# Optimization experiments

Measured on AMD Instinct MI355X. Metric: run time of the kernel, lower is better.

Reference implementation:

```python
import jax, jax.numpy as jnp
import numpy as np

B, N, M = 64, 4096, 128


def setup_inputs() -> dict:
    key = jax.random.key(0)
    x = jax.random.normal(key, (B, N, M), dtype=jnp.float32)
    return {"x": x}


def reference(x):
    # Original loops over channels M, applying a 1D FFT along the N axis to
    # each (batch, N) slice. Equivalent batched form: FFT along axis=1.
    f = jnp.fft.fft(x.astype(jnp.complex64), axis=1)  # (B, N, M) complex64
    return (jnp.real(f), jnp.imag(f))
```

## Files before the change

### kernel.cpp

```cpp
#include <hip/hip_runtime.h>
#include <hip/hip_fp16.h>

#define B 64
#define N 4096
#define M 128

constexpr int T    = 1024;
constexpr int CPB  = 16;
constexpr int NF   = 8;
constexpr int NWG  = B * (M / CPB);

__device__ __forceinline__ int fold5(int p) {
    return (p & ~31) | ((p ^ (p >> 5) ^ (p >> 9)) & 31);
}
__device__ __forceinline__ int rev12(int k) {
    return ((k & 7) << 9) | (((k >> 3) & 7) << 6) | (((k >> 6) & 7) << 3) | ((k >> 9) & 7);
}

__device__ __forceinline__ float2 cadd(float2 a, float2 b){ return make_float2(a.x+b.x, a.y+b.y); }
__device__ __forceinline__ float2 csub(float2 a, float2 b){ return make_float2(a.x-b.x, a.y-b.y); }
__device__ __forceinline__ float2 cmul(float2 a, float2 b){ return make_float2(a.x*b.x - a.y*b.y, a.x*b.y + a.y*b.x); }
__device__ __forceinline__ float2 mulnegi(float2 a){ return make_float2(a.y, -a.x); }
__device__ __forceinline__ float2 muli(float2 a)  { return make_float2(-a.y, a.x); }
__device__ __forceinline__ float2 cis(float ang){ float s, c; __sincosf(ang, &s, &c); return make_float2(c, s); }
__device__ __forceinline__ float2 h2f(__half2 h){ return __half22float2(h); }
__device__ __forceinline__ __half2 f2h(float2 v){ return __floats2half2_rn(v.x, v.y); }

__device__ __forceinline__ void dft8(float2 t[8]) {
    float2 e0=cadd(t[0],t[4]), e1=csub(t[0],t[4]);
    float2 e2=cadd(t[2],t[6]), e3=csub(t[2],t[6]);
    float2 E0=cadd(e0,e2), E2=csub(e0,e2);
    float2 E1=cadd(e1,mulnegi(e3)), E3=cadd(e1,muli(e3));
    float2 o0=cadd(t[1],t[5]), o1=csub(t[1],t[5]);
    float2 o2=cadd(t[3],t[7]), o3=csub(t[3],t[7]);
    float2 O0=cadd(o0,o2), O2=csub(o0,o2);
    float2 O1=cadd(o1,mulnegi(o3)), O3=cadd(o1,muli(o3));
    const float C = 0.70710678118654752f;
    float2 w1O1 = make_float2(C*(O1.x+O1.y), C*(O1.y-O1.x));
    float2 w2O2 = mulnegi(O2);
    float2 w3O3 = make_float2(C*(O3.y-O3.x), -C*(O3.x+O3.y));
    t[0]=cadd(E0,O0);   t[4]=csub(E0,O0);
    t[1]=cadd(E1,w1O1); t[5]=csub(E1,w1O1);
    t[2]=cadd(E2,w2O2); t[6]=csub(E2,w2O2);
    t[3]=cadd(E3,w3O3); t[7]=csub(E3,w3O3);
}

template<int S>
__device__ __forceinline__ void stage(__half2* z, int tid) {
    #pragma unroll
    for (int it = 0; it < 4; ++it) {
        const int q  = tid + (it << 10);
        const int f  = q >> 9;
        const int qq = q & 511;
        int G, j;
        if      (S == 512) { G = 0;                j = qq;      }
        else if (S == 64)  { G = (qq >> 6) << 9;   j = qq & 63; }
        else if (S == 8)   { G = (qq >> 3) << 6;   j = qq & 7;  }
        else               { G = qq << 3;          j = 0;       }
        const int nbase = G + j;
        const int fb = f << 12;
        int idx[8];
        #pragma unroll
        for (int c = 0; c < 8; ++c) idx[c] = fb + fold5(nbase + c * S);
        float2 r[8];
        #pragma unroll
        for (int c = 0; c < 8; ++c) r[c] = h2f(z[idx[c]]);
        dft8(r);
        if (S > 1) {
            float2 w1 = cis(-6.2831853071795864f * (float)j / (float)(8 * S));
            float2 w = w1;
            #pragma unroll
            for (int k = 1; k < 8; ++k) { r[k] = cmul(r[k], w); w = cmul(w, w1); }
        }
        #pragma unroll
        for (int c = 0; c < 8; ++c) z[idx[c]] = f2h(r[c]);
    }
}

__global__ __launch_bounds__(T, 4)
void fft_one(const float* __restrict__ x, float* __restrict__ out) {
    extern __shared__ __half2 z[];
    const int bid = blockIdx.x;
    const int b = bid >> 3, mg = bid & 7;
    const int m0 = mg * CPB;
    const float* xb = x + (size_t)b * N * M + m0;
    const int tid = threadIdx.x;

    #pragma unroll
    for (int it = 0; it < 16; ++it) {
        int i = tid + (it << 10);
        int n = i >> 2, c = i & 3;
        float4 v = *(const float4*)(xb + (size_t)n * M + (c << 2));
        int fn = fold5(n);
        z[((2 * c)     << 12) + fn] = f2h(make_float2(v.x, v.y));
        z[((2 * c + 1) << 12) + fn] = f2h(make_float2(v.z, v.w));
    }
    __syncthreads();

    stage<512>(z, tid); __syncthreads();
    stage<64 >(z, tid); __syncthreads();
    stage<8  >(z, tid); __syncthreads();
    stage<1  >(z, tid); __syncthreads();

    float* outRe = out;
    float* outIm = out + (size_t)B * N * M;
    const size_t rbase = (size_t)b * N * M + m0;
    #pragma unroll
    for (int it = 0; it < 16; ++it) {
        int u = tid + (it << 10);
        int k = u >> 2, c = u & 3;
        int kk = (N - k) & (N - 1);
        int sk = fold5(rev12(k)), smk = fold5(rev12(kk));
        int f0 = (2 * c) << 12, f1 = (2 * c + 1) << 12;
        float2 Zk0 = h2f(z[f0 + sk]),  Zm0 = h2f(z[f0 + smk]);
        float2 Zk1 = h2f(z[f1 + sk]),  Zm1 = h2f(z[f1 + smk]);
        float4 re, im;
        re.x = 0.5f * (Zk0.x + Zm0.x); im.x = 0.5f * (Zk0.y - Zm0.y);
        re.y = 0.5f * (Zk0.y + Zm0.y); im.y = 0.5f * (Zm0.x - Zk0.x);
        re.z = 0.5f * (Zk1.x + Zm1.x); im.z = 0.5f * (Zk1.y - Zm1.y);
        re.w = 0.5f * (Zk1.y + Zm1.y); im.w = 0.5f * (Zm1.x - Zk1.x);
        *(float4*)(outRe + rbase + (size_t)k * M + (c << 2)) = re;
        *(float4*)(outIm + rbase + (size_t)k * M + (c << 2)) = im;
    }
}

extern "C" void kernel_launch(void* const* d_in, const int* in_sizes, int n_in,
                              void* d_out, int out_size, void* d_ws, size_t ws_size,
                              hipStream_t stream) {
    const float* x = (const float*)d_in[0];
    float* out = (float*)d_out;
    const int lds_bytes = NF * N * (int)sizeof(__half2);
    hipFuncSetAttribute((const void*)fft_one,
                        hipFuncAttributeMaxDynamicSharedMemorySize, lds_bytes);
    fft_one<<<NWG, T, lds_bytes, stream>>>(x, out);
}
```

Baseline: 146.1 us.

## Replace four-stage LDS radix-8 FFT with register-resident 64x64 four-step FFT

Restructures the 4096-point FFT as a 64x64 four-step decomposition. Each thread does two 64-point FFTs in registers, with twiddle multiplication in between and a single LDS transpose using an XOR-swizzled layout. This replaces four LDS round-trip stages and their barriers. Global loads become float2 strided reads loaded straight into registers, and the block is 512 threads with a remapped block-to-batch order. The risk is heavy register pressure (64+64 float2 arrays) that may cause spills, plus narrower, less coalesced global accesses.

```diff
diff --git a/kernel.cpp b/kernel.cpp
--- a/kernel.cpp
+++ b/kernel.cpp
@@ -5,17 +5,8 @@
 #define N 4096
 #define M 128
 
-constexpr int T    = 1024;
-constexpr int CPB  = 16;
-constexpr int NF   = 8;
-constexpr int NWG  = B * (M / CPB);
-
-__device__ __forceinline__ int fold5(int p) {
-    return (p & ~31) | ((p ^ (p >> 5) ^ (p >> 9)) & 31);
-}
-__device__ __forceinline__ int rev12(int k) {
-    return ((k & 7) << 9) | (((k >> 3) & 7) << 6) | (((k >> 6) & 7) << 3) | ((k >> 9) & 7);
-}
+constexpr int T   = 512;
+constexpr int NWG = 512;
 
 __device__ __forceinline__ float2 cadd(float2 a, float2 b){ return make_float2(a.x+b.x, a.y+b.y); }
 __device__ __forceinline__ float2 csub(float2 a, float2 b){ return make_float2(a.x-b.x, a.y-b.y); }
@@ -45,82 +36,102 @@
     t[3]=cadd(E3,w3O3); t[7]=csub(E3,w3O3);
 }
 
-template<int S>
-__device__ __forceinline__ void stage(__half2* z, int tid) {
+__device__ __forceinline__ void fft64(float2 z[64]) {
+    float2 y[64];
     #pragma unroll
-    for (int it = 0; it < 4; ++it) {
-        const int q  = tid + (it << 10);
-        const int f  = q >> 9;
-        const int qq = q & 511;
-        int G, j;
-        if      (S == 512) { G = 0;                j = qq;      }
-        else if (S == 64)  { G = (qq >> 6) << 9;   j = qq & 63; }
-        else if (S == 8)   { G = (qq >> 3) << 6;   j = qq & 7;  }
-        else               { G = qq << 3;          j = 0;       }
-        const int nbase = G + j;
-        const int fb = f << 12;
-        int idx[8];
+    for (int bb = 0; bb < 8; ++bb) {
+        float2 t[8];
         #pragma unroll
-        for (int c = 0; c < 8; ++c) idx[c] = fb + fold5(nbase + c * S);
-        float2 r[8];
+        for (int a = 0; a < 8; ++a) t[a] = z[8*a+bb];
+        dft8(t);
         #pragma unroll
-        for (int c = 0; c < 8; ++c) r[c] = h2f(z[idx[c]]);
-        dft8(r);
-        if (S > 1) {
-            float2 w1 = cis(-6.2831853071795864f * (float)j / (float)(8 * S));
+        for (int d = 0; d < 8; ++d) y[8*bb+d] = t[d];
+    }
+    #pragma unroll
+    for (int d = 0; d < 8; ++d) {
+        float2 t[8];
+        #pragma unroll
+        for (int bb = 0; bb < 8; ++bb) t[bb] = y[8*bb+d];
+        if (d > 0) {
+            float2 w1 = cis(-6.2831853071795864f * (float)d / 64.0f);
             float2 w = w1;
             #pragma unroll
-            for (int k = 1; k < 8; ++k) { r[k] = cmul(r[k], w); w = cmul(w, w1); }
+            for (int bb = 1; bb < 8; ++bb) { t[bb] = cmul(t[bb], w); w = cmul(w, w1); }
         }
+        dft8(t);
         #pragma unroll
-        for (int c = 0; c < 8; ++c) z[idx[c]] = f2h(r[c]);
+        for (int c = 0; c < 8; ++c) z[8*c+d] = t[c];
     }
 }
 
-__global__ __launch_bounds__(T, 4)
+__device__ __forceinline__ int lslot(int k1, int n2, int mc) {
+    return (k1 << 9) | ((n2 ^ (k1 & 7)) << 3) | mc;
+}
+
+__global__ __launch_bounds__(T, 2)
 void fft_one(const float* __restrict__ x, float* __restrict__ out) {
-    extern __shared__ __half2 z[];
+    extern __shared__ __half2 lz[];
+
     const int bid = blockIdx.x;
-    const int b = bid >> 3, mg = bid & 7;
-    const int m0 = mg * CPB;
-    const float* xb = x + (size_t)b * N * M + m0;
+    const int b   = ((bid >> 6) << 3) | (bid & 7);
+    const int mcg = (bid >> 3) & 7;
     const int tid = threadIdx.x;
+    const int mc  = tid & 7;
+    const int rp  = tid >> 3;
+
+    const float* xb = x + (size_t)b * N * M + mcg * 16 + mc * 2;
+
+    float2 z[64];
+    #pragma unroll
+    for (int n1 = 0; n1 < 64; ++n1)
+        z[n1] = *(const float2*)(xb + (size_t)(64 * n1 + rp) * M);
+    fft64(z);
+
+    {
+        float2 ws = cis(-6.2831853071795864f * (float)rp / 4096.0f);
+        float2 pw[8];
+        pw[0] = make_float2(1.f, 0.f);
+        #pragma unroll
+        for (int d = 1; d < 8; ++d) pw[d] = cmul(pw[d-1], ws);
+        float2 w8 = cmul(pw[7], ws);
+        float2 ac = make_float2(1.f, 0.f);
+        #pragma unroll
+        for (int c = 0; c < 8; ++c) {
+            #pragma unroll
+            for (int d = 0; d < 8; ++d)
+                z[8*c+d] = cmul(z[8*c+d], cmul(ac, pw[d]));
+            ac = cmul(ac, w8);
+        }
+    }
 
     #pragma unroll
-    for (int it = 0; it < 16; ++it) {
-        int i = tid + (it << 10);
-        int n = i >> 2, c = i & 3;
-        float4 v = *(const float4*)(xb + (size_t)n * M + (c << 2));
-        int fn = fold5(n);
-        z[((2 * c)     << 12) + fn] = f2h(make_float2(v.x, v.y));
-        z[((2 * c + 1) << 12) + fn] = f2h(make_float2(v.z, v.w));
-    }
+    for (int k1 = 0; k1 < 64; ++k1)
+        lz[lslot(k1, rp, mc)] = f2h(z[k1]);
     __syncthreads();
 
-    stage<512>(z, tid); __syncthreads();
-    stage<64 >(z, tid); __syncthreads();
-    stage<8  >(z, tid); __syncthreads();
-    stage<1  >(z, tid); __syncthreads();
+    #pragma unroll
+    for (int n2 = 0; n2 < 64; ++n2)
+        z[n2] = h2f(lz[lslot(rp, n2, mc)]);
+    fft64(z);
+    #pragma unroll
+    for (int k2 = 0; k2 < 64; ++k2)
+        lz[lslot(rp, k2, mc)] = f2h(z[k2]);
+    __syncthreads();
 
-    float* outRe = out;
-    float* outIm = out + (size_t)B * N * M;
-    const size_t rbase = (size_t)b * N * M + m0;
-    #pragma unroll
-    for (int it = 0; it < 16; ++it) {
-        int u = tid + (it << 10);
-        int k = u >> 2, c = u & 3;
-        int kk = (N - k) & (N - 1);
-        int sk = fold5(rev12(k)), smk = fold5(rev12(kk));
-        int f0 = (2 * c) << 12, f1 = (2 * c + 1) << 12;
-        float2 Zk0 = h2f(z[f0 + sk]),  Zm0 = h2f(z[f0 + smk]);
-        float2 Zk1 = h2f(z[f1 + sk]),  Zm1 = h2f(z[f1 + smk]);
-        float4 re, im;
-        re.x = 0.5f * (Zk0.x + Zm0.x); im.x = 0.5f * (Zk0.y - Zm0.y);
-        re.y = 0.5f * (Zk0.y + Zm0.y); im.y = 0.5f * (Zm0.x - Zk0.x);
-        re.z = 0.5f * (Zk1.x + Zm1.x); im.z = 0.5f * (Zk1.y - Zm1.y);
-        re.w = 0.5f * (Zk1.y + Zm1.y); im.w = 0.5f * (Zm1.x - Zk1.x);
-        *(float4*)(outRe + rbase + (size_t)k * M + (c << 2)) = re;
-        *(float4*)(outIm + rbase + (size_t)k * M + (c << 2)) = im;
+    float* outRe = out + (size_t)b * N * M + mcg * 16 + mc * 2;
+    float* outIm = outRe + (size_t)B * N * M;
+    const int r = rp;
+    #pragma unroll 4
+    for (int j = 0; j < 64; ++j) {
+        int k   = (j << 6) | r;
+        int kk  = (N - k) & (N - 1);
+        int k1p = kk & 63, k2p = kk >> 6;
+        float2 Zk = h2f(lz[lslot(r,   j,   mc)]);
+        float2 Zm = h2f(lz[lslot(k1p, k2p, mc)]);
+        float2 re = make_float2(0.5f * (Zk.x + Zm.x), 0.5f * (Zk.y + Zm.y));
+        float2 im = make_float2(0.5f * (Zk.y - Zm.y), 0.5f * (Zm.x - Zk.x));
+        *(float2*)(outRe + (size_t)k * M) = re;
+        *(float2*)(outIm + (size_t)k * M) = im;
     }
 }
 
@@ -129,7 +140,7 @@
                               hipStream_t stream) {
     const float* x = (const float*)d_in[0];
     float* out = (float*)d_out;
-    const int lds_bytes = NF * N * (int)sizeof(__half2);
+    const int lds_bytes = 64 * 64 * 8 * (int)sizeof(__half2);
     hipFuncSetAttribute((const void*)fft_one,
                         hipFuncAttributeMaxDynamicSharedMemorySize, lds_bytes);
     fft_one<<<NWG, T, lds_bytes, stream>>>(x, out);
```

New measurement: 189.2 us. 29.5% more time.
